# Kernel optimization log

Measured on AMD Instinct MI355X. Metric: run time of the kernel, lower is better.

## Reference

```python
import jax, jax.numpy as jnp
import numpy as np

HEAD_SIZE = 256
ROTARY_DIM = 64
ROPE_THETA = 10000.0


def apply_gptj_rope(x, positions):
    """GPT-J (interleaved, non-neox) rotary embedding.
    x: [B, S, H, D], positions: [B, S] int. Rotates first ROTARY_DIM dims."""
    half = ROTARY_DIM // 2
    inv_freq = 1.0 / (ROPE_THETA ** (jnp.arange(0, ROTARY_DIM, 2, dtype=jnp.float32) / ROTARY_DIM))
    ang = positions.astype(jnp.float32)[..., None] * inv_freq      # [B, S, half]
    cos = jnp.cos(ang)[:, :, None, :]                               # [B, S, 1, half]
    sin = jnp.sin(ang)[:, :, None, :]
    xr, xp = x[..., :ROTARY_DIM], x[..., ROTARY_DIM:]
    x1, x2 = xr[..., 0::2], xr[..., 1::2]                           # interleaved pairs
    o1 = x1 * cos - x2 * sin
    o2 = x2 * cos + x1 * sin
    rot = jnp.stack([o1, o2], axis=-1).reshape(*xr.shape)           # re-interleave
    return jnp.concatenate([rot, xp], axis=-1)


def setup_inputs() -> dict:
    key = jax.random.key(0)
    k1, k2, k3 = jax.random.split(key, 3)
    B, S, H = 2, 2048, 4096
    position_ids = jnp.broadcast_to(jnp.arange(S, dtype=jnp.int32), (B, S))
    hidden_states = jax.random.normal(k1, (B, S, H), dtype=jnp.float32)
    Wqkv = jax.random.normal(k2, (H, 3 * H), dtype=jnp.float32) * (H ** -0.5)
    Wo = jax.random.normal(k3, (H, H), dtype=jnp.float32) * (H ** -0.5)
    return {"position_ids": position_ids, "hidden_states": hidden_states, "Wqkv": Wqkv, "Wo": Wo}


def reference(position_ids, hidden_states, Wqkv, Wo):
    B, S, H = hidden_states.shape
    nh = H // HEAD_SIZE
    qkv = hidden_states @ Wqkv                                      # [B, S, 3H]
    q, k, v = jnp.split(qkv, 3, axis=-1)
    q = apply_gptj_rope(q.reshape(B, S, nh, HEAD_SIZE), position_ids)
    k = apply_gptj_rope(k.reshape(B, S, nh, HEAD_SIZE), position_ids)
    v = v.reshape(B, S, nh, HEAD_SIZE)
    scale = HEAD_SIZE ** -0.5
    scores = jnp.einsum('bqhd,bkhd->bhqk', q, k) * scale            # [B, nh, S, S]
    causal = jnp.tril(jnp.ones((S, S), dtype=bool))
    scores = jnp.where(causal, scores, jnp.finfo(scores.dtype).min)
    attn = jax.nn.softmax(scores, axis=-1)
    ctx = jnp.einsum('bhqk,bkhd->bqhd', attn, v).reshape(B, S, H)
    return ctx @ Wo
```

## Files before the change

kernel.cpp:

```cpp
#include <hip/hip_runtime.h>
#include <hip/hip_bf16.h>

typedef __bf16 bf16x8 __attribute__((ext_vector_type(8)));
typedef float f32x4 __attribute__((ext_vector_type(4)));

#define MFMA_BF16(a,b,c) __builtin_amdgcn_mfma_f32_16x16x32_bf16(a,b,c,0,0,0)

#define GLOAD16(g, l) __builtin_amdgcn_global_load_lds( \
    (const __attribute__((address_space(1))) unsigned int*)(g), \
    (__attribute__((address_space(3))) unsigned int*)(l), 16, 0, 0)

__device__ __forceinline__ unsigned short f2bf(float f) {
  unsigned u = __builtin_bit_cast(unsigned, f);
  return (unsigned short)((u + 0x7FFFu + ((u >> 16) & 1u)) >> 16);
}

__global__ __launch_bounds__(256)
void convert_bf16(const float* __restrict__ src, unsigned short* __restrict__ dst,
                  int n8) {
  int i = blockIdx.x * blockDim.x + threadIdx.x;
  int stride = gridDim.x * blockDim.x;
  for (; i < n8; i += stride) {
    float4 a = ((const float4*)src)[i*2];
    float4 b = ((const float4*)src)[i*2 + 1];
    short4 h0, h1;
    h0.x = (short)f2bf(a.x); h0.y = (short)f2bf(a.y);
    h0.z = (short)f2bf(a.z); h0.w = (short)f2bf(a.w);
    h1.x = (short)f2bf(b.x); h1.y = (short)f2bf(b.y);
    h1.z = (short)f2bf(b.z); h1.w = (short)f2bf(b.w);
    ((short4*)dst)[i*2] = h0;
    ((short4*)dst)[i*2 + 1] = h1;
  }
}

__global__ __launch_bounds__(256)
void transpose_convert(const float* __restrict__ W, unsigned short* __restrict__ Wt,
                       int K, int N) {
  __shared__ float tl[64][65];
  const int k0 = blockIdx.y * 64, n0 = blockIdx.x * 64;
  const int tr = threadIdx.x >> 4;
  const int tc4 = (threadIdx.x & 15) * 4;
  for (int i = 0; i < 4; ++i) {
    int r = tr + i*16;
    float4 v = *(const float4*)(W + (size_t)(k0 + r)*N + n0 + tc4);
    tl[r][tc4+0] = v.x; tl[r][tc4+1] = v.y;
    tl[r][tc4+2] = v.z; tl[r][tc4+3] = v.w;
  }
  __syncthreads();
  for (int i = 0; i < 4; ++i) {
    int nr = tr + i*16;
    short4 h;
    h.x = (short)f2bf(tl[tc4+0][nr]);
    h.y = (short)f2bf(tl[tc4+1][nr]);
    h.z = (short)f2bf(tl[tc4+2][nr]);
    h.w = (short)f2bf(tl[tc4+3][nr]);
    *(short4*)(Wt + (size_t)(n0 + nr)*K + k0 + tc4) = h;
  }
}

__global__ __launch_bounds__(256)
void transpose_v(const unsigned short* __restrict__ qkv,
                 unsigned short* __restrict__ Vt) {
  __shared__ unsigned short tl[64][68];
  const int bh = blockIdx.z;
  const int s0 = blockIdx.x * 64;
  const int d0 = blockIdx.y * 64;
  const int b = bh >> 4, h = bh & 15;
  const int tr = threadIdx.x >> 4;
  const int tc = (threadIdx.x & 15) * 4;
  const unsigned short* src = qkv + ((size_t)(b*2048 + s0))*12288 + 8192 + h*256 + d0;
  for (int i = 0; i < 4; ++i) {
    int s = tr + i*16;
    *(short4*)&tl[s][tc] = *(const short4*)(src + (size_t)s*12288 + tc);
  }
  __syncthreads();
  unsigned short* dst = Vt + ((size_t)bh*256 + d0)*2048 + s0;
  for (int i = 0; i < 4; ++i) {
    int d = tr + i*16;
    short4 h4;
    h4.x = (short)tl[tc+0][d];
    h4.y = (short)tl[tc+1][d];
    h4.z = (short)tl[tc+2][d];
    h4.w = (short)tl[tc+3][d];
    *(short4*)(dst + (size_t)d*2048 + tc) = h4;
  }
}

template<bool ROPE, bool OUT_BF16>
__global__ __launch_bounds__(512, 2)
void gemm256p(const unsigned short* __restrict__ A,
              const unsigned short* __restrict__ Bt,
              const int* __restrict__ pos,
              void* __restrict__ Cp, int N, int K, int nbx)
{
  __shared__ __align__(16) unsigned short L[2][4][8192];
  const int tid = threadIdx.x, lane = tid & 63, w = tid >> 6;
  const int wr = w >> 2, wc = w & 3;
  const int nwg = gridDim.x;
  int wg = blockIdx.x;
  if ((nwg & 7) == 0) wg = (wg & 7) * (nwg >> 3) + (wg >> 3);
  const int bx = wg % nbx, by = wg / nbx;
  const int row0 = by * 256, col0 = bx * 256;

  const int crow = lane & 15, g = lane >> 4;
  const int xo = (crow & 7) << 4;
  const int rB0 = (wc & 1) * 64;
  const unsigned bo = (unsigned)((tid >> 3) * K + (((tid & 7) ^ ((tid >> 3) & 7)) * 8));
  const int nt = K >> 6;

#define STG_A(T,BUF,H,RLO) do { if ((T) < nt)                                   \
    GLOAD16(A + (unsigned)((row0 + (H)*128 + (RLO))*K) + bo + (unsigned)(T)*64u,\
            &L[BUF][H][(RLO)*64 + tid*8]); } while (0)
#define STG_B(T,BUF,H,RLO) do { if ((T) < nt)                                   \
    GLOAD16(Bt + (unsigned)((col0 + (H)*128 + (RLO))*K) + bo + (unsigned)(T)*64u,\
            &L[BUF][2+(H)][(RLO)*64 + tid*8]); } while (0)

#define RD_ALO(BUF) _Pragma("unroll") for (int m = 0; m < 4; ++m)               \
    _Pragma("unroll") for (int kk = 0; kk < 2; ++kk)                            \
      pAlo[m][kk] = *(const bf16x8*)((const char*)&L[BUF][wr][0] +              \
                     (m*16 + crow)*128 + ((((kk*4+g)<<4)) ^ xo));
#define RD_AHI(BUF) _Pragma("unroll") for (int m = 0; m < 4; ++m)               \
    _Pragma("unroll") for (int kk = 0; kk < 2; ++kk)                            \
      pAhi[m][kk] = *(const bf16x8*)((const char*)&L[BUF][wr][0] +              \
                     (64 + m*16 + crow)*128 + ((((kk*4+g)<<4)) ^ xo));
#define RD_B0(BUF) _Pragma("unroll") for (int n = 0; n < 2; ++n)                \
    _Pragma("unroll") for (int kk = 0; kk < 2; ++kk)                            \
      pB0[n][kk] = *(const bf16x8*)((const char*)&L[BUF][2+(wc>>1)][0] +        \
                    (rB0 + n*16 + crow)*128 + ((((kk*4+g)<<4)) ^ xo));
#define RD_B1(BUF) _Pragma("unroll") for (int n = 0; n < 2; ++n)                \
    _Pragma("unroll") for (int kk = 0; kk < 2; ++kk)                            \
      pB1[n][kk] = *(const bf16x8*)((const char*)&L[BUF][2+(wc>>1)][0] +        \
                    (rB0 + 32 + n*16 + crow)*128 + ((((kk*4+g)<<4)) ^ xo));
#define Q00 _Pragma("unroll") for (int kk = 0; kk < 2; ++kk)                    \
    _Pragma("unroll") for (int m = 0; m < 4; ++m)                               \
    _Pragma("unroll") for (int n = 0; n < 2; ++n)                               \
      acc[m][n] = MFMA_BF16(pAlo[m][kk], pB0[n][kk], acc[m][n]);
#define Q01 _Pragma("unroll") for (int kk = 0; kk < 2; ++kk)                    \
    _Pragma("unroll") for (int m = 0; m < 4; ++m)                               \
    _Pragma("unroll") for (int n = 0; n < 2; ++n)                               \
      acc[m][2+n] = MFMA_BF16(pAlo[m][kk], pB1[n][kk], acc[m][2+n]);
#define Q10 _Pragma("unroll") for (int kk = 0; kk < 2; ++kk)                    \
    _Pragma("unroll") for (int m = 0; m < 4; ++m)                               \
    _Pragma("unroll") for (int n = 0; n < 2; ++n)                               \
      acc[4+m][n] = MFMA_BF16(pAhi[m][kk], pB0[n][kk], acc[4+m][n]);
#define Q11 _Pragma("unroll") for (int kk = 0; kk < 2; ++kk)                    \
    _Pragma("unroll") for (int m = 0; m < 4; ++m)                               \
    _Pragma("unroll") for (int n = 0; n < 2; ++n)                               \
      acc[4+m][2+n] = MFMA_BF16(pAhi[m][kk], pB1[n][kk], acc[4+m][2+n]);
#define BAR __builtin_amdgcn_s_barrier()
#define LGKM0 asm volatile("s_waitcnt lgkmcnt(0)" ::: "memory")
#define LGKM8 asm volatile("s_waitcnt lgkmcnt(8)" ::: "memory")
#define PRIO1 __builtin_amdgcn_s_setprio(1)
#define PRIO0 __builtin_amdgcn_s_setprio(0)

  f32x4 acc[8][4] = {};
  STG_A(0,0,0,0);  STG_A(0,0,0,64); STG_A(0,0,1,0);  STG_A(0,0,1,64);
  STG_B(0,0,0,0);  STG_B(0,0,0,64); STG_B(0,0,1,0);  STG_B(0,0,1,64);
  STG_A(1,1,0,0);  STG_A(1,1,1,0);
  STG_B(1,1,0,0);  STG_B(1,1,0,64); STG_B(1,1,1,0);  STG_B(1,1,1,64);
  asm volatile("s_waitcnt vmcnt(6)" ::: "memory");
  BAR;

  const int nI = nt >> 1;
  for (int i = 0; i < nI; ++i) {
    const int t = 2*i;
    const bool last = (i == nI - 1);
    bf16x8 pAlo[4][2], pAhi[4][2], pB0[2][2], pB1[2][2];

    RD_ALO(0); RD_B0(0);
    STG_A(t+1, 1, 0, 64); STG_A(t+1, 1, 1, 64);
    LGKM8;
    BAR; LGKM0; PRIO1; Q00; PRIO0; BAR;
    RD_B1(0);
    STG_A(t+2, 0, 0, 0); STG_A(t+2, 0, 1, 0);
    BAR; LGKM0; PRIO1; Q01; PRIO0; BAR;
    RD_AHI(0);
    STG_B(t+2, 0, 0, 0); STG_B(t+2, 0, 0, 64);
    BAR; LGKM0; PRIO1; Q10; PRIO0; BAR;
    STG_B(t+2, 0, 1, 0); STG_B(t+2, 0, 1, 64);
    PRIO1; Q11; PRIO0;
    if (!last) asm volatile("s_waitcnt vmcnt(6)" ::: "memory");
    else       asm volatile("s_waitcnt vmcnt(0)" ::: "memory");
    BAR;

    RD_ALO(1); RD_B0(1);
    STG_A(t+2, 0, 0, 64); STG_A(t+2, 0, 1, 64);
    LGKM8;
    BAR; LGKM0; PRIO1; Q00; PRIO0; BAR;
    RD_B1(1);
    STG_A(t+3, 1, 0, 0); STG_A(t+3, 1, 1, 0);
    BAR; LGKM0; PRIO1; Q01; PRIO0; BAR;
    RD_AHI(1);
    STG_B(t+3, 1, 0, 0); STG_B(t+3, 1, 0, 64);
    BAR; LGKM0; PRIO1; Q10; PRIO0; BAR;
    STG_B(t+3, 1, 1, 0); STG_B(t+3, 1, 1, 64);
    PRIO1; Q11; PRIO0;
    if (!last) asm volatile("s_waitcnt vmcnt(6)" ::: "memory");
    else       asm volatile("s_waitcnt vmcnt(0)" ::: "memory");
    BAR;
  }
#undef STG_A
#undef STG_B
#undef RD_ALO
#undef RD_AHI
#undef RD_B0
#undef RD_B1
#undef Q00
#undef Q01
#undef Q10
#undef Q11
#undef BAR
#undef LGKM0
#undef LGKM8
#undef PRIO1
#undef PRIO0

#pragma unroll
  for (int m = 0; m < 8; ++m) {
    const int rbase = row0 + wr*128 + m*16 + (g << 2);
#pragma unroll
    for (int n = 0; n < 4; ++n) {
      const int c = col0 + wc*64 + n*16 + crow;
      bool rot = false;
      float invf = 0.f;
      if (ROPE) {
        rot = (c < 8192) && ((c & 255) < 64);
        if (rot) {
          int i2 = (c & 63) >> 1;
          invf = exp2f(-(float)i2 * 0.4152410118609203f);
        }
      }
#pragma unroll
      for (int r = 0; r < 4; ++r) {
        int rowg = rbase + r;
        float v = acc[m][n][r];
        if (ROPE && rot) {
          float ang = (float)pos[rowg] * invf;
          float s_ = __sinf(ang), c_ = __cosf(ang);
          float pv = __shfl_xor(v, 1, 64);
          v = (c & 1) ? fmaf(v, c_, pv * s_) : fmaf(v, c_, -pv * s_);
        }
        if (OUT_BF16)
          ((unsigned short*)Cp)[(size_t)rowg*N + c] = f2bf(v);
        else
          ((float*)Cp)[(size_t)rowg*N + c] = v;
      }
    }
  }
}

template<bool A_BF16, bool ROPE, bool OUT_BF16>
__global__ __launch_bounds__(256)
void gemm128(const void* __restrict__ Ap, const float* __restrict__ Bp,
             const int* __restrict__ pos, void* __restrict__ Cp,
             int N, int K)
{
  __shared__ __align__(16) short Al[128*40];
  __shared__ __align__(16) short Bl[128*40];
  const int tid = threadIdx.x;
  const int lane = tid & 63, wid = tid >> 6;
  const int wr = wid >> 1, wc = wid & 1;
  const int row0 = blockIdx.y * 128, col0 = blockIdx.x * 128;
  f32x4 acc[4][4] = {};
  const int bcol = tid & 127;
  const int kb0 = (tid >> 7) * 4;

  for (int kt = 0; kt < K; kt += 32) {
    if (A_BF16) {
      const unsigned short* Ab = (const unsigned short*)Ap;
      for (int i = 0; i < 2; ++i) {
        int idx = tid + i*256;
        int ar = idx >> 2, ac = (idx & 3) * 8;
        *(int4*)(&Al[ar*40 + ac]) = *(const int4*)(Ab + (size_t)(row0+ar)*K + kt + ac);
      }
    } else {
      const float* Af = (const float*)Ap;
      for (int i = 0; i < 4; ++i) {
        int idx = tid + i*256;
        int ar = idx >> 3, ac = (idx & 7) * 4;
        float4 v = *(const float4*)(Af + (size_t)(row0+ar)*K + kt + ac);
        short4 h;
        h.x = (short)f2bf(v.x); h.y = (short)f2bf(v.y);
        h.z = (short)f2bf(v.z); h.w = (short)f2bf(v.w);
        *(short4*)(&Al[ar*40 + ac]) = h;
      }
    }
    for (int r = 0; r < 4; ++r) {
      int kb = kb0 + r*8;
      const float* bp = Bp + (size_t)(kt+kb)*N + col0 + bcol;
      float x0 = bp[0];
      float x1 = bp[(size_t)N];
      float x2 = bp[2*(size_t)N];
      float x3 = bp[3*(size_t)N];
      short4 h;
      h.x = (short)f2bf(x0); h.y = (short)f2bf(x1);
      h.z = (short)f2bf(x2); h.w = (short)f2bf(x3);
      *(short4*)(&Bl[bcol*40 + kb]) = h;
    }
    __syncthreads();
    const int k8 = (lane >> 4) * 8;
    bf16x8 af[4], bfr[4];
    for (int m = 0; m < 4; ++m)
      af[m] = *(const bf16x8*)(&Al[(wr*64 + m*16 + (lane&15))*40 + k8]);
    for (int n = 0; n < 4; ++n)
      bfr[n] = *(const bf16x8*)(&Bl[(wc*64 + n*16 + (lane&15))*40 + k8]);
    for (int m = 0; m < 4; ++m)
      for (int n = 0; n < 4; ++n)
        acc[m][n] = MFMA_BF16(af[m], bfr[n], acc[m][n]);
    __syncthreads();
  }

  for (int m = 0; m < 4; ++m) {
    const int rbase = row0 + wr*64 + m*16 + ((lane>>4)<<2);
    for (int n = 0; n < 4; ++n) {
      const int c = col0 + wc*64 + n*16 + (lane & 15);
      bool rot = false;
      float invf = 0.f;
      if (ROPE) {
        rot = (c < 8192) && ((c & 255) < 64);
        if (rot) {
          int i2 = (c & 63) >> 1;
          invf = exp2f(-(float)i2 * 0.4152410118609203f);
        }
      }
      for (int r = 0; r < 4; ++r) {
        int rowg = rbase + r;
        float v = acc[m][n][r];
        if (ROPE && rot) {
          float ang = (float)pos[rowg] * invf;
          float s_ = __sinf(ang), c_ = __cosf(ang);
          float pv = __shfl_xor(v, 1, 64);
          v = (c & 1) ? fmaf(v, c_, pv * s_) : fmaf(v, c_, -pv * s_);
        }
        if (OUT_BF16)
          ((unsigned short*)Cp)[(size_t)rowg*N + c] = f2bf(v);
        else
          ((float*)Cp)[(size_t)rowg*N + c] = v;
      }
    }
  }
}

__global__ __launch_bounds__(512, 2)
void attn_kernel3(const unsigned short* __restrict__ qkv,
                  const unsigned short* __restrict__ Vt,
                  unsigned short* __restrict__ ctx)
{
  const int QN = 12288;
  __shared__ __align__(16) unsigned char Kl[2][32768];
  __shared__ __align__(16) unsigned char Vl[2][32768];
  __shared__ __align__(16) unsigned char Pl[128*144];
  const int tid = threadIdx.x, lane = tid & 63, w = tid >> 6;
  const int qp = blockIdx.x, bh = blockIdx.y;
  const int b = bh >> 4, h = bh & 15;
  const size_t rowbase = (size_t)b * 2048;
  const int colr = lane & 15, g = lane >> 4;

  const int kr0 = tid >> 5;
  const int kcolb = ((tid*16) & 511) ^ ((kr0 & 7) << 4);
  const unsigned koff = (unsigned)(kr0*QN) + (kcolb >> 1);
  const int vd0 = tid >> 3;
  const int vcolb = ((tid*16) & 127) ^ ((vd0 & 7) << 4);
  const unsigned voff = (unsigned)(vd0*2048) + (vcolb >> 1);

  const unsigned short* kbase = qkv + rowbase*QN + 4096 + h*256;
  const unsigned short* vbase = Vt + (size_t)bh*256*2048;

#define STAGEKV(KT, B) do {                                                    \
    const unsigned short* kb_ = kbase + (unsigned)(KT)*64u*(unsigned)QN;       \
    const unsigned short* vb_ = vbase + (unsigned)(KT)*64u;                    \
    _Pragma("unroll")                                                          \
    for (int i = 0; i < 4; ++i)                                                \
      GLOAD16(kb_ + koff + i*16*QN, &Kl[B][tid*16 + i*8192]);                  \
    _Pragma("unroll")                                                          \
    for (int i = 0; i < 4; ++i)                                                \
      GLOAD16(vb_ + voff + i*64*2048, &Vl[B][tid*16 + i*8192]);                \
  } while (0)

  for (int phase = 0; phase < 2; ++phase) {
    const int qt = phase ? qp : (15 - qp);
    const int nkt = 2*qt + 2;

    bf16x8 qf[8];
    {
      const unsigned short* qp_ = qkv + (rowbase + qt*128 + w*16 + colr)*QN + h*256 + g*8;
#pragma unroll
      for (int f = 0; f < 8; ++f)
        qf[f] = *(const bf16x8*)(qp_ + 32*f);
    }
    f32x4 acc[16] = {};
    float m_r[4], l_r[4];
#pragma unroll
    for (int r = 0; r < 4; ++r) { m_r[r] = -1e30f; l_r[r] = 0.f; }

    STAGEKV(0, 0);
    STAGEKV(1, 1);
    int cur = 0;

    for (int kt = 0; kt < nkt; ++kt) {
      if (kt < nkt - 1) asm volatile("s_waitcnt vmcnt(8)" ::: "memory");
      else              asm volatile("s_waitcnt vmcnt(0)" ::: "memory");
      __builtin_amdgcn_s_barrier();

      const unsigned char* Kb = Kl[cur];
      f32x4 sc[4];
      __builtin_amdgcn_s_setprio(1);
#pragma unroll
      for (int nf = 0; nf < 4; ++nf) {
        f32x4 s = {};
        int krow = nf*16 + colr;
        int xo2 = (krow & 7) << 4;
        const unsigned char* kp = Kb + krow*512;
#pragma unroll
        for (int st = 0; st < 8; ++st) {
          bf16x8 kf = *(const bf16x8*)(kp + ((64*st + 16*g) ^ xo2));
          s = MFMA_BF16(qf[st], kf, s);
        }
        sc[nf] = s;
      }
      __builtin_amdgcn_s_setprio(0);

      const int qrow0 = qt*128 + w*16 + g*4;
      float pm[4] = {-3e38f,-3e38f,-3e38f,-3e38f};
      float pvv[4][4];
#pragma unroll
      for (int nf = 0; nf < 4; ++nf) {
        int kcol = kt*64 + nf*16 + colr;
#pragma unroll
        for (int r = 0; r < 4; ++r) {
          float v = sc[nf][r] * 0.0625f;
          if (kcol > qrow0 + r) v = -1e30f;
          pvv[nf][r] = v;
          pm[r] = fmaxf(pm[r], v);
        }
      }
#pragma unroll
      for (int mk = 1; mk < 16; mk <<= 1)
#pragma unroll
        for (int r = 0; r < 4; ++r)
          pm[r] = fmaxf(pm[r], __shfl_xor(pm[r], mk, 64));
      float alpha[4];
#pragma unroll
      for (int r = 0; r < 4; ++r) {
        float mn = fmaxf(m_r[r], pm[r]);
        alpha[r] = __expf(m_r[r] - mn);
        m_r[r] = mn;
      }
      float ps[4] = {0.f,0.f,0.f,0.f};
      unsigned short pb[4][4];
#pragma unroll
      for (int nf = 0; nf < 4; ++nf)
#pragma unroll
        for (int r = 0; r < 4; ++r) {
          float p = __expf(pvv[nf][r] - m_r[r]);
          ps[r] += p;
          pb[nf][r] = f2bf(p);
        }
#pragma unroll
      for (int mk = 1; mk < 16; mk <<= 1)
#pragma unroll
        for (int r = 0; r < 4; ++r)
          ps[r] += __shfl_xor(ps[r], mk, 64);
#pragma unroll
      for (int r = 0; r < 4; ++r)
        l_r[r] = l_r[r]*alpha[r] + ps[r];
#pragma unroll
      for (int nf2 = 0; nf2 < 16; ++nf2)
#pragma unroll
        for (int r = 0; r < 4; ++r)
          acc[nf2][r] *= alpha[r];

#pragma unroll
      for (int nf = 0; nf < 4; ++nf)
#pragma unroll
        for (int r = 0; r < 4; ++r)
          *(unsigned short*)(Pl + (w*16 + g*4 + r)*144 + (nf*16 + colr)*2) = pb[nf][r];

      const unsigned char* Vb = Vl[cur];
      __builtin_amdgcn_s_setprio(1);
#pragma unroll
      for (int st2 = 0; st2 < 2; ++st2) {
        bf16x8 pf = *(const bf16x8*)(Pl + (w*16 + colr)*144 + (32*st2 + g*8)*2);
#pragma unroll
        for (int nf2 = 0; nf2 < 16; ++nf2) {
          int d = nf2*16 + colr;
          bf16x8 vf = *(const bf16x8*)(Vb + ((d*128 + 64*st2 + 16*g) ^ ((d&7)<<4)));
          acc[nf2] = MFMA_BF16(pf, vf, acc[nf2]);
        }
      }
      __builtin_amdgcn_s_setprio(0);

      __builtin_amdgcn_sched_barrier(0);
      asm volatile("s_waitcnt lgkmcnt(0)" ::: "memory");
      __builtin_amdgcn_sched_barrier(0);
      __builtin_amdgcn_s_barrier();
      if (kt + 2 < nkt) STAGEKV(kt + 2, cur);
      cur ^= 1;
    }

    float linv[4];
#pragma unroll
    for (int r = 0; r < 4; ++r) linv[r] = 1.0f / l_r[r];
#pragma unroll
    for (int nf2 = 0; nf2 < 16; ++nf2)
#pragma unroll
      for (int r = 0; r < 4; ++r) {
        int qrow = qt*128 + w*16 + g*4 + r;
        float o = acc[nf2][r] * linv[r];
        ctx[(rowbase + qrow)*4096 + h*256 + nf2*16 + colr] = f2bf(o);
      }
  }
#undef STAGEKV
}

__global__ __launch_bounds__(256, 2)
void attn_kernel2(const unsigned short* __restrict__ qkv,
                  unsigned short* __restrict__ ctx)
{
  const int S = 2048, D = 256, QN = 12288;
  __shared__ __align__(16) unsigned char Kl[64*512];
  __shared__ __align__(16) unsigned char Vl[256*128];
  __shared__ __align__(16) unsigned char Pl[64*144];
  const int tid = threadIdx.x, lane = tid & 63, w = tid >> 6;
  const int qp = blockIdx.x, bh = blockIdx.y;
  const int b = bh >> 4, h = bh & 15;
  const size_t rowbase = (size_t)b * S;
  const int colr = lane & 15, g = lane >> 4;

  const int kr0 = tid >> 5, c8 = (tid & 31) * 8;
  const unsigned kwb = (unsigned)((kr0*512 + c8*2) ^ ((kr0 & 7) << 4));
  const int dd = (tid >> 2) * 4, kbb = (tid & 3) * 4;

  const unsigned short* kbase0 = qkv + rowbase*QN + 4096 + h*D;
  const unsigned short* vbase0 = qkv + rowbase*QN + 8192 + h*D;

  bf16x8 kreg[8];
  short4 vreg[16];

#define LOADKV(KT) do {                                                        \
    const unsigned short* kb_ = kbase0 + (size_t)(KT)*64*QN;                   \
    _Pragma("unroll")                                                          \
    for (int i = 0; i < 8; ++i)                                                \
      kreg[i] = *(const bf16x8*)(kb_ + (size_t)(kr0 + i*8)*QN + c8);           \
    const unsigned short* vb_ = vbase0 + (size_t)(KT)*64*QN;                   \
    _Pragma("unroll")                                                          \
    for (int r4 = 0; r4 < 4; ++r4) {                                           \
      int kb2 = kbb + 16*r4;                                                   \
      _Pragma("unroll")                                                        \
      for (int j = 0; j < 4; ++j)                                              \
        vreg[r4*4+j] = *(const short4*)(vb_ + (size_t)(kb2+j)*QN + dd);        \
    }                                                                          \
  } while (0)

#define WRITEKV() do {                                                         \
    _Pragma("unroll")                                                          \
    for (int i = 0; i < 8; ++i)                                                \
      *(bf16x8*)(Kl + kwb + i*4096) = kreg[i];                                 \
    _Pragma("unroll")                                                          \
    for (int r4 = 0; r4 < 4; ++r4) {                                           \
      int kb2 = kbb + 16*r4;                                                   \
      short4 v0 = vreg[r4*4+0], v1 = vreg[r4*4+1];                             \
      short4 v2 = vreg[r4*4+2], v3 = vreg[r4*4+3];                             \
      short4 t;                                                                \
      t.x=v0.x; t.y=v1.x; t.z=v2.x; t.w=v3.x;                                  \
      *(short4*)(Vl + (((dd+0)*128 + kb2*2) ^ (((dd+0)&7)<<4))) = t;           \
      t.x=v0.y; t.y=v1.y; t.z=v2.y; t.w=v3.y;                                  \
      *(short4*)(Vl + (((dd+1)*128 + kb2*2) ^ (((dd+1)&7)<<4))) = t;           \
      t.x=v0.z; t.y=v1.z; t.z=v2.z; t.w=v3.z;                                  \
      *(short4*)(Vl + (((dd+2)*128 + kb2*2) ^ (((dd+2)&7)<<4))) = t;           \
      t.x=v0.w; t.y=v1.w; t.z=v2.w; t.w=v3.w;                                  \
      *(short4*)(Vl + (((dd+3)*128 + kb2*2) ^ (((dd+3)&7)<<4))) = t;           \
    }                                                                          \
  } while (0)

  for (int phase = 0; phase < 2; ++phase) {
    const int qt = phase ? qp : (31 - qp);

    bf16x8 qf[8];
    {
      const unsigned short* qp_ = qkv + (rowbase + qt*64 + w*16 + colr)*QN + h*D + g*8;
#pragma unroll
      for (int f = 0; f < 8; ++f)
        qf[f] = *(const bf16x8*)(qp_ + 32*f);
    }
    f32x4 acc[16] = {};
    float m_r[4], l_r[4];
#pragma unroll
    for (int r = 0; r < 4; ++r) { m_r[r] = -1e30f; l_r[r] = 0.f; }

    LOADKV(0);
    WRITEKV();
    __syncthreads();

    for (int kt = 0; kt <= qt; ++kt) {
      if (kt < qt) LOADKV(kt + 1);
      __builtin_amdgcn_sched_barrier(0);

      f32x4 sc[4];
#pragma unroll
      for (int nf = 0; nf < 4; ++nf) {
        f32x4 s = {};
        int krow = nf*16 + colr;
        int xo2 = (krow & 7) << 4;
        const unsigned char* kp = Kl + krow*512;
#pragma unroll
        for (int st = 0; st < 8; ++st) {
          bf16x8 kf = *(const bf16x8*)(kp + ((64*st + 16*g) ^ xo2));
          s = MFMA_BF16(qf[st], kf, s);
        }
        sc[nf] = s;
      }

      const int qrow0 = qt*64 + w*16 + g*4;
      float pm[4] = {-3e38f,-3e38f,-3e38f,-3e38f};
      float pvv[4][4];
#pragma unroll
      for (int nf = 0; nf < 4; ++nf) {
        int kcol = kt*64 + nf*16 + colr;
#pragma unroll
        for (int r = 0; r < 4; ++r) {
          float v = sc[nf][r] * 0.0625f;
          if (kcol > qrow0 + r) v = -1e30f;
          pvv[nf][r] = v;
          pm[r] = fmaxf(pm[r], v);
        }
      }
#pragma unroll
      for (int mk = 1; mk < 16; mk <<= 1)
#pragma unroll
        for (int r = 0; r < 4; ++r)
          pm[r] = fmaxf(pm[r], __shfl_xor(pm[r], mk, 64));
      float alpha[4];
#pragma unroll
      for (int r = 0; r < 4; ++r) {
        float mn = fmaxf(m_r[r], pm[r]);
        alpha[r] = __expf(m_r[r] - mn);
        m_r[r] = mn;
      }
      float ps[4] = {0.f,0.f,0.f,0.f};
      unsigned short pb[4][4];
#pragma unroll
      for (int nf = 0; nf < 4; ++nf)
#pragma unroll
        for (int r = 0; r < 4; ++r) {
          float p = __expf(pvv[nf][r] - m_r[r]);
          ps[r] += p;
          pb[nf][r] = f2bf(p);
        }
#pragma unroll
      for (int mk = 1; mk < 16; mk <<= 1)
#pragma unroll
        for (int r = 0; r < 4; ++r)
          ps[r] += __shfl_xor(ps[r], mk, 64);
#pragma unroll
      for (int r = 0; r < 4; ++r)
        l_r[r] = l_r[r]*alpha[r] + ps[r];
#pragma unroll
      for (int nf2 = 0; nf2 < 16; ++nf2)
#pragma unroll
        for (int r = 0; r < 4; ++r)
          acc[nf2][r] *= alpha[r];

#pragma unroll
      for (int nf = 0; nf < 4; ++nf)
#pragma unroll
        for (int r = 0; r < 4; ++r)
          *(unsigned short*)(Pl + (w*16 + g*4 + r)*144 + (nf*16 + colr)*2) = pb[nf][r];

#pragma unroll
      for (int st2 = 0; st2 < 2; ++st2) {
        bf16x8 pf = *(const bf16x8*)(Pl + (w*16 + colr)*144 + (32*st2 + g*8)*2);
#pragma unroll
        for (int nf2 = 0; nf2 < 16; ++nf2) {
          int d = nf2*16 + colr;
          bf16x8 vf = *(const bf16x8*)(Vl + ((d*128 + 64*st2 + 16*g) ^ ((d&7)<<4)));
          acc[nf2] = MFMA_BF16(pf, vf, acc[nf2]);
        }
      }
      __syncthreads();
      if (kt < qt) {
        WRITEKV();
        __syncthreads();
      }
    }

    float linv[4];
#pragma unroll
    for (int r = 0; r < 4; ++r) linv[r] = 1.0f / l_r[r];
#pragma unroll
    for (int nf2 = 0; nf2 < 16; ++nf2)
#pragma unroll
      for (int r = 0; r < 4; ++r) {
        int qrow = qt*64 + w*16 + g*4 + r;
        float o = acc[nf2][r] * linv[r];
        ctx[(rowbase + qrow)*4096 + h*D + nf2*16 + colr] = f2bf(o);
      }
    if (phase == 0) __syncthreads();
  }
#undef LOADKV
#undef WRITEKV
}

extern "C" void kernel_launch(void* const* d_in, const int* in_sizes, int n_in,
                              void* d_out, int out_size, void* d_ws, size_t ws_size,
                              hipStream_t stream) {
  const int*   pos    = (const int*)d_in[0];
  const float* hidden = (const float*)d_in[1];
  const float* Wqkv   = (const float*)d_in[2];
  const float* Wo     = (const float*)d_in[3];

  const size_t QKV_B  = (size_t)4096 * 12288 * 2;
  const size_t CTX_B  = (size_t)4096 * 4096 * 2;
  const size_t FAST_NEED = QKV_B + QKV_B + CTX_B;

  if (ws_size >= FAST_NEED) {
    unsigned short* qkv     = (unsigned short*)d_ws;
    unsigned short* WqkvT   = (unsigned short*)((char*)d_ws + QKV_B);
    unsigned short* WoT     = WqkvT;
    unsigned short* ctx     = (unsigned short*)((char*)d_ws + QKV_B + CTX_B);
    unsigned short* hiddenB = (unsigned short*)((char*)d_ws + 2*QKV_B);
    unsigned short* Vt      = hiddenB;

    convert_bf16<<<2048, 256, 0, stream>>>(hidden, hiddenB, 4096*4096/8);
    transpose_convert<<<dim3(192, 64), 256, 0, stream>>>(Wqkv, WqkvT, 4096, 12288);
    gemm256p<true, true><<<768, 512, 0, stream>>>(
        hiddenB, WqkvT, pos, qkv, 12288, 4096, 48);
    transpose_convert<<<dim3(64, 64), 256, 0, stream>>>(Wo, WoT, 4096, 4096);
    transpose_v<<<dim3(32, 4, 32), 256, 0, stream>>>(qkv, Vt);
    attn_kernel3<<<dim3(8, 32), 512, 0, stream>>>(qkv, Vt, ctx);
    gemm256p<false, false><<<256, 512, 0, stream>>>(
        ctx, WoT, nullptr, d_out, 4096, 4096, 16);
  } else {
    if (ws_size < QKV_B + CTX_B) return;
    unsigned short* qkv = (unsigned short*)d_ws;
    unsigned short* ctx = qkv + (size_t)4096 * 12288;
    gemm128<false, true, true><<<dim3(96, 32), 256, 0, stream>>>(
        hidden, Wqkv, pos, qkv, 12288, 4096);
    attn_kernel2<<<dim3(16, 32), 256, 0, stream>>>(qkv, ctx);
    gemm128<true, false, false><<<dim3(32, 32), 256, 0, stream>>>(
        ctx, Wo, nullptr, d_out, 4096, 4096);
  }
}
```

Measured before the change: 734.6 us.

## Fuse V transpose into QKV GEMM epilogue and merge prep conversions

Merges the hidden-state bf16 conversion and the Wqkv transpose-convert into a single launch. When enough workspace exists, the QKV GEMM epilogue writes V tiles directly in transposed layout to a separate buffer, removing the transpose_v kernel and its extra read/write of V. The transposed stores are strided short4 writes, which may coalesce poorly, and the fused path depends on extra workspace being available.

```diff
diff --git a/kernel.cpp b/kernel.cpp
--- a/kernel.cpp
+++ b/kernel.cpp
@@ -16,20 +16,46 @@
 }
 
 __global__ __launch_bounds__(256)
-void convert_bf16(const float* __restrict__ src, unsigned short* __restrict__ dst,
-                  int n8) {
-  int i = blockIdx.x * blockDim.x + threadIdx.x;
-  int stride = gridDim.x * blockDim.x;
-  for (; i < n8; i += stride) {
-    float4 a = ((const float4*)src)[i*2];
-    float4 b = ((const float4*)src)[i*2 + 1];
-    short4 h0, h1;
-    h0.x = (short)f2bf(a.x); h0.y = (short)f2bf(a.y);
-    h0.z = (short)f2bf(a.z); h0.w = (short)f2bf(a.w);
-    h1.x = (short)f2bf(b.x); h1.y = (short)f2bf(b.y);
-    h1.z = (short)f2bf(b.z); h1.w = (short)f2bf(b.w);
-    ((short4*)dst)[i*2] = h0;
-    ((short4*)dst)[i*2 + 1] = h1;
+void prep_merged(const float* __restrict__ hidden, unsigned short* __restrict__ hiddenB,
+                 const float* __restrict__ Wqkv, unsigned short* __restrict__ WqkvT) {
+  __shared__ float tl[64][65];
+  const int id = blockIdx.x;
+  if (id < 12288) {
+    const int n0 = (id % 192) * 64, k0 = (id / 192) * 64;
+    const int K = 4096, N = 12288;
+    const int tr = threadIdx.x >> 4;
+    const int tc4 = (threadIdx.x & 15) * 4;
+    for (int i = 0; i < 4; ++i) {
+      int r = tr + i*16;
+      float4 v = *(const float4*)(Wqkv + (size_t)(k0 + r)*N + n0 + tc4);
+      tl[r][tc4+0] = v.x; tl[r][tc4+1] = v.y;
+      tl[r][tc4+2] = v.z; tl[r][tc4+3] = v.w;
+    }
+    __syncthreads();
+    for (int i = 0; i < 4; ++i) {
+      int nr = tr + i*16;
+      short4 h;
+      h.x = (short)f2bf(tl[tc4+0][nr]);
+      h.y = (short)f2bf(tl[tc4+1][nr]);
+      h.z = (short)f2bf(tl[tc4+2][nr]);
+      h.w = (short)f2bf(tl[tc4+3][nr]);
+      *(short4*)(WqkvT + (size_t)(n0 + nr)*K + k0 + tc4) = h;
+    }
+  } else {
+    const int n8 = 4096*4096/8;
+    int i = (id - 12288) * 256 + threadIdx.x;
+    const int stride = 2048 * 256;
+    for (; i < n8; i += stride) {
+      float4 a = ((const float4*)hidden)[i*2];
+      float4 b = ((const float4*)hidden)[i*2 + 1];
+      short4 h0, h1;
+      h0.x = (short)f2bf(a.x); h0.y = (short)f2bf(a.y);
+      h0.z = (short)f2bf(a.z); h0.w = (short)f2bf(a.w);
+      h1.x = (short)f2bf(b.x); h1.y = (short)f2bf(b.y);
+      h1.z = (short)f2bf(b.z); h1.w = (short)f2bf(b.w);
+      ((short4*)hiddenB)[i*2] = h0;
+      ((short4*)hiddenB)[i*2 + 1] = h1;
+    }
   }
 }
 
@@ -86,12 +112,13 @@
   }
 }
 
-template<bool ROPE, bool OUT_BF16>
+template<bool ROPE, bool OUT_BF16, bool VFUSE>
 __global__ __launch_bounds__(512, 2)
 void gemm256p(const unsigned short* __restrict__ A,
               const unsigned short* __restrict__ Bt,
               const int* __restrict__ pos,
-              void* __restrict__ Cp, int N, int K, int nbx)
+              void* __restrict__ Cp, int N, int K, int nbx,
+              unsigned short* __restrict__ Vt)
 {
   __shared__ __align__(16) unsigned short L[2][4][8192];
   const int tid = threadIdx.x, lane = tid & 63, w = tid >> 6;
@@ -215,6 +242,25 @@
 #undef PRIO1
 #undef PRIO0
 
+  if (VFUSE && ROPE && col0 >= 8192) {
+#pragma unroll
+    for (int m = 0; m < 8; ++m) {
+      const int rbase = row0 + wr*128 + m*16 + (g << 2);
+      const int b = rbase >> 11, s0 = rbase & 2047;
+#pragma unroll
+      for (int n = 0; n < 4; ++n) {
+        const int d = col0 - 8192 + wc*64 + n*16 + crow;
+        short4 hv;
+        hv.x = (short)f2bf(acc[m][n][0]);
+        hv.y = (short)f2bf(acc[m][n][1]);
+        hv.z = (short)f2bf(acc[m][n][2]);
+        hv.w = (short)f2bf(acc[m][n][3]);
+        *(short4*)(Vt + ((size_t)(b*4096 + d))*2048 + s0) = hv;
+      }
+    }
+    return;
+  }
+
 #pragma unroll
   for (int m = 0; m < 8; ++m) {
     const int rbase = row0 + wr*128 + m*16 + (g << 2);
@@ -711,6 +757,7 @@
 
   const size_t QKV_B  = (size_t)4096 * 12288 * 2;
   const size_t CTX_B  = (size_t)4096 * 4096 * 2;
+  const size_t VT_B   = (size_t)32 * 256 * 2048 * 2;
   const size_t FAST_NEED = QKV_B + QKV_B + CTX_B;
 
   if (ws_size >= FAST_NEED) {
@@ -719,17 +766,24 @@
     unsigned short* WoT     = WqkvT;
     unsigned short* ctx     = (unsigned short*)((char*)d_ws + QKV_B + CTX_B);
     unsigned short* hiddenB = (unsigned short*)((char*)d_ws + 2*QKV_B);
-    unsigned short* Vt      = hiddenB;
-
-    convert_bf16<<<2048, 256, 0, stream>>>(hidden, hiddenB, 4096*4096/8);
-    transpose_convert<<<dim3(192, 64), 256, 0, stream>>>(Wqkv, WqkvT, 4096, 12288);
-    gemm256p<true, true><<<768, 512, 0, stream>>>(
-        hiddenB, WqkvT, pos, qkv, 12288, 4096, 48);
+
+    const bool vfuse = ws_size >= FAST_NEED + VT_B;
+    unsigned short* Vt = vfuse ? (unsigned short*)((char*)d_ws + FAST_NEED)
+                               : hiddenB;
+
+    prep_merged<<<14336, 256, 0, stream>>>(hidden, hiddenB, Wqkv, WqkvT);
+    if (vfuse)
+      gemm256p<true, true, true><<<768, 512, 0, stream>>>(
+          hiddenB, WqkvT, pos, qkv, 12288, 4096, 48, Vt);
+    else
+      gemm256p<true, true, false><<<768, 512, 0, stream>>>(
+          hiddenB, WqkvT, pos, qkv, 12288, 4096, 48, nullptr);
     transpose_convert<<<dim3(64, 64), 256, 0, stream>>>(Wo, WoT, 4096, 4096);
-    transpose_v<<<dim3(32, 4, 32), 256, 0, stream>>>(qkv, Vt);
+    if (!vfuse)
+      transpose_v<<<dim3(32, 4, 32), 256, 0, stream>>>(qkv, Vt);
     attn_kernel3<<<dim3(8, 32), 512, 0, stream>>>(qkv, Vt, ctx);
-    gemm256p<false, false><<<256, 512, 0, stream>>>(
-        ctx, WoT, nullptr, d_out, 4096, 4096, 16);
+    gemm256p<false, false, false><<<256, 512, 0, stream>>>(
+        ctx, WoT, nullptr, d_out, 4096, 4096, 16, nullptr);
   } else {
     if (ws_size < QKV_B + CTX_B) return;
     unsigned short* qkv = (unsigned short*)d_ws;
```

After: 723.7 us. No clear change (-1.5%).
